# Kernel tuning notes

Measured on AMD Instinct MI355X. Metric: run time of the kernel, lower is better.

Reference implementation:

```python
import jax, jax.numpy as jnp
import numpy as np

NUM_NODES = 100000
NODE_FEAT_DIM = 512
EDGE_FEAT_DIM = 512
MEM_DIM = NODE_FEAT_DIM + EDGE_FEAT_DIM  # 1024
BATCH = 65536


def setup_inputs() -> dict:
    key = jax.random.key(0)
    k_ids, k_mem, k_emb, kq, ks, kk = jax.random.split(key, 6)
    scale = 1.0 / np.sqrt(MEM_DIM)
    inp = {
        "node_ids": jax.random.randint(k_ids, (BATCH,), 0, NUM_NODES, dtype=jnp.int64)
        if jax.config.jax_enable_x64 else
        jax.random.randint(k_ids, (BATCH,), 0, NUM_NODES, dtype=jnp.int32),
        # memory bank: (N, 1, D); randomized (instead of the zero init) so math is non-trivial
        "node_memories": jax.random.normal(k_mem, (NUM_NODES, 1, MEM_DIM), dtype=jnp.float32) * 0.02,
        "node_embedding": jax.random.normal(k_emb, (NUM_NODES, MEM_DIM), dtype=jnp.float32) * 0.02,
        "Wq": jax.random.normal(jax.random.fold_in(kq, 0), (MEM_DIM, NODE_FEAT_DIM), dtype=jnp.float32) * scale,
        "bq": jnp.zeros((NODE_FEAT_DIM,), dtype=jnp.float32),
        "Ws": jax.random.normal(jax.random.fold_in(ks, 0), (MEM_DIM, NODE_FEAT_DIM), dtype=jnp.float32) * scale,
        "bs": jnp.zeros((NODE_FEAT_DIM,), dtype=jnp.float32),
        "Wk": jax.random.normal(jax.random.fold_in(kk, 0), (MEM_DIM, NODE_FEAT_DIM), dtype=jnp.float32) * scale,
        "bk": jnp.zeros((NODE_FEAT_DIM,), dtype=jnp.float32),
    }
    return inp


def reference(node_ids, node_memories, node_embedding, Wq, bq, Ws, bs, Wk, bk):
    ids = node_ids.astype(jnp.int32)
    # torch.sum(node_memories[ids], dim=2): reduces feature dim -> (B, 1)
    mem_sum = jnp.sum(node_memories[ids], axis=2)          # (B, 1)
    x = mem_sum + node_embedding[ids]                      # broadcast -> (B, D)
    q = jax.nn.sigmoid(x @ Wq + bq)                        # (B, node_feat_dim)
    s = jax.nn.sigmoid(x @ Ws + bs)
    k = jax.nn.sigmoid(x @ Wk + bk)
    return (q, s, k)
```

## Files before the change

kernel.cpp:

```cpp
#include <hip/hip_runtime.h>
#include <hip/hip_bf16.h>
#include <stdint.h>

#define BATCH_N 65536
#define KDIM 1024
#define NTOT 1536

typedef __bf16 bf16x8 __attribute__((ext_vector_type(8)));
typedef float f32x4 __attribute__((ext_vector_type(4)));

__device__ __forceinline__ unsigned short f2bf(float f) {
    unsigned u = __builtin_bit_cast(unsigned, f);
    u += 0x7FFFu + ((u >> 16) & 1u);
    return (unsigned short)(u >> 16);
}

__global__ __launch_bounds__(256) void prep_kernel(
    const int* __restrict__ ids,
    const float* __restrict__ mem,
    const float* __restrict__ emb,
    unsigned short* __restrict__ x)
{
    const int b    = blockIdx.x * 4 + (threadIdx.x >> 6);
    const int lane = threadIdx.x & 63;
    const int id   = ids[b];
    const float4* m4 = (const float4*)(mem + (size_t)id * KDIM) + lane;
    const float4* e4 = (const float4*)(emb + (size_t)id * KDIM) + lane;
    float4 v0 = m4[0];
    float4 v1 = m4[64];
    float4 v2 = m4[128];
    float4 v3 = m4[192];
    float s = (v0.x + v0.y + v0.z + v0.w) + (v1.x + v1.y + v1.z + v1.w)
            + (v2.x + v2.y + v2.z + v2.w) + (v3.x + v3.y + v3.z + v3.w);
    #pragma unroll
    for (int off = 1; off < 64; off <<= 1) s += __shfl_xor(s, off, 64);
    unsigned short* xb = x + (size_t)b * KDIM;
    #pragma unroll
    for (int q = 0; q < 4; ++q) {
        float4 e = e4[q * 64];
        ushort4 o;
        o.x = f2bf(s + e.x);
        o.y = f2bf(s + e.y);
        o.z = f2bf(s + e.z);
        o.w = f2bf(s + e.w);
        const int k   = q * 256 + lane * 4;
        const int ksw = k ^ ((b & 7) << 3);
        *(ushort4*)(xb + ksw) = o;
    }
}

__global__ __launch_bounds__(256) void wconv_kernel(
    const float* __restrict__ Wq, const float* __restrict__ Ws,
    const float* __restrict__ Wk, unsigned short* __restrict__ wt)
{
    const int gt = blockIdx.x * 256 + threadIdx.x;
    const int n  = gt % NTOT;
    const int kb = (gt / NTOT) * 4;
    const float* W = (n < 512) ? Wq : ((n < 1024) ? Ws : Wk);
    const int nn = n & 511;
    ushort4 o;
    o.x = f2bf(W[(size_t)(kb + 0) * 512 + nn]);
    o.y = f2bf(W[(size_t)(kb + 1) * 512 + nn]);
    o.z = f2bf(W[(size_t)(kb + 2) * 512 + nn]);
    o.w = f2bf(W[(size_t)(kb + 3) * 512 + nn]);
    const int ksw = kb ^ ((n & 7) << 3);
    *(ushort4*)(wt + (size_t)n * KDIM + ksw) = o;
}

#define BM 256
#define BN 256
#define BK 64
#define MT (BATCH_N / BM)
#define NT (NTOT / BN)
#define NWG (MT * NT)

#define BAR() asm volatile("s_barrier" ::: "memory")
#define LGKM0() asm volatile("s_waitcnt lgkmcnt(0)" ::: "memory")
#define VM6() asm volatile("s_waitcnt vmcnt(6)" ::: "memory")
#define VM0() asm volatile("s_waitcnt vmcnt(0)" ::: "memory")
#define AS1 __attribute__((address_space(1)))
#define AS3 __attribute__((address_space(3)))

__global__ __launch_bounds__(512, 2) void gemm_kernel(
    const unsigned short* __restrict__ X,
    const unsigned short* __restrict__ Wt,
    const float* __restrict__ bq, const float* __restrict__ bs,
    const float* __restrict__ bk, float* __restrict__ out)
{
    __shared__ __align__(16) unsigned short sA[32768];
    __shared__ __align__(16) unsigned short sB[32768];

    const int tid  = threadIdx.x;
    const int xcd  = blockIdx.x & 7;
    const int idx  = blockIdx.x >> 3;
    const int wgid = xcd * (NWG / 8) + idx;
    const int nt   = wgid % NT;
    const int mt   = wgid / NT;
    const int m0   = mt * BM;
    const int n0   = nt * BN;
    const int wid  = tid >> 6;
    const int lane = tid & 63;
    const int wm   = wid >> 2;
    const int wn   = wid & 3;
    const int r16  = lane & 15;
    const int kb0  = (lane >> 4) << 4;
    const int ksw  = (r16 & 7) << 4;

    f32x4 acc[8][4];
    #pragma unroll
    for (int i = 0; i < 8; i++)
        #pragma unroll
        for (int j = 0; j < 4; j++)
            acc[i][j] = f32x4{0.f, 0.f, 0.f, 0.f};

    bf16x8 af[4][2], bfr0[2][2], bfr1[2][2];

    const unsigned short* gA = X  + (size_t)(m0 + (tid >> 3)) * KDIM + (tid & 7) * 8;
    const unsigned short* gB = Wt + (size_t)(n0 + (tid >> 3)) * KDIM + (tid & 7) * 8;
    const int ldst = (tid & 448) * 8;

#define STG_A(slot, h, kt) do {                                                 \
    _Pragma("unroll")                                                            \
    for (int c = 0; c < 2; ++c)                                                  \
        __builtin_amdgcn_global_load_lds(                                        \
            (const AS1 void*)(gA + (size_t)((h) * 128 + c * 64) * KDIM + (kt) * BK), \
            (AS3 void*)(&sA[((slot) * 2 + (h)) * 8192 + c * 4096 + ldst]),       \
            16, 0, 0);                                                           \
} while (0)
#define STG_B(slot, h, kt) do {                                                 \
    _Pragma("unroll")                                                            \
    for (int c = 0; c < 2; ++c)                                                  \
        __builtin_amdgcn_global_load_lds(                                        \
            (const AS1 void*)(gB + (size_t)((h) * 128 + c * 64) * KDIM + (kt) * BK), \
            (AS3 void*)(&sB[((slot) * 2 + (h)) * 8192 + c * 4096 + ldst]),       \
            16, 0, 0);                                                           \
} while (0)

#define LDA(slot, qa) do {                                                      \
    const char* p = (const char*)&sA[((slot) * 2 + (qa)) * 8192];                \
    _Pragma("unroll")                                                            \
    for (int i = 0; i < 4; ++i)                                                  \
        _Pragma("unroll")                                                        \
        for (int kk = 0; kk < 2; ++kk)                                           \
            af[i][kk] = *(const bf16x8*)(p + (wm * 64 + i * 16 + r16) * 128      \
                                           + ((kk * 64 + kb0) ^ ksw));           \
} while (0)
#define LDB(slot, qb, SET) do {                                                 \
    const char* p = (const char*)&sB[((slot) * 2 + (qb)) * 8192];                \
    _Pragma("unroll")                                                            \
    for (int j = 0; j < 2; ++j)                                                  \
        _Pragma("unroll")                                                        \
        for (int kk = 0; kk < 2; ++kk)                                           \
            SET[j][kk] = *(const bf16x8*)(p + (wn * 32 + j * 16 + r16) * 128     \
                                            + ((kk * 64 + kb0) ^ ksw));          \
} while (0)

#define MM(QA, QB, SET) do {                                                    \
    __builtin_amdgcn_s_setprio(1);                                               \
    _Pragma("unroll")                                                            \
    for (int i = 0; i < 4; ++i)                                                  \
        _Pragma("unroll")                                                        \
        for (int j = 0; j < 2; ++j)                                              \
            _Pragma("unroll")                                                    \
            for (int kk = 0; kk < 2; ++kk)                                       \
                acc[(QA) * 4 + i][(QB) * 2 + j] =                                \
                    __builtin_amdgcn_mfma_f32_16x16x32_bf16(                     \
                        af[i][kk], SET[j][kk], acc[(QA) * 4 + i][(QB) * 2 + j],  \
                        0, 0, 0);                                                \
    __builtin_amdgcn_s_setprio(0);                                               \
} while (0)

    STG_A(0, 0, 0); STG_A(0, 1, 0); STG_B(0, 0, 0); STG_B(0, 1, 0);
    STG_A(1, 0, 1); STG_B(1, 1, 1); STG_A(1, 1, 1);
    VM0();
    BAR();

    #pragma unroll 1
    for (int t = 0; t < 7; ++t) {
        const int ka = 2 * t + 1, kb2 = 2 * t + 2, kc = 2 * t + 3;
        LDA(0, 0); LDB(0, 0, bfr0); STG_B(1, 0, ka);
        BAR(); LGKM0(); MM(0, 0, bfr0); BAR();
        LDB(0, 1, bfr1); STG_A(0, 0, kb2);
        BAR(); LGKM0(); MM(0, 1, bfr1); BAR();
        LDA(0, 1); STG_B(0, 1, kb2);
        BAR(); LGKM0(); MM(1, 1, bfr1); BAR();
        STG_A(0, 1, kb2);
        BAR(); LGKM0(); MM(1, 0, bfr0); VM6(); BAR();
        LDA(1, 0); LDB(1, 0, bfr0); STG_B(0, 0, kb2);
        BAR(); LGKM0(); MM(0, 0, bfr0); BAR();
        LDB(1, 1, bfr1); STG_A(1, 0, kc);
        BAR(); LGKM0(); MM(0, 1, bfr1); BAR();
        LDA(1, 1); STG_B(1, 1, kc);
        BAR(); LGKM0(); MM(1, 1, bfr1); BAR();
        STG_A(1, 1, kc);
        BAR(); LGKM0(); MM(1, 0, bfr0); VM6(); BAR();
    }
    LDA(0, 0); LDB(0, 0, bfr0); STG_B(1, 0, 15);
    BAR(); LGKM0(); MM(0, 0, bfr0); BAR();
    LDB(0, 1, bfr1);
    BAR(); LGKM0(); MM(0, 1, bfr1); BAR();
    LDA(0, 1);
    BAR(); LGKM0(); MM(1, 1, bfr1); BAR();
    BAR(); LGKM0(); MM(1, 0, bfr0); VM0(); BAR();
    LDA(1, 0); LDB(1, 0, bfr0);
    BAR(); LGKM0(); MM(0, 0, bfr0); BAR();
    LDB(1, 1, bfr1);
    BAR(); LGKM0(); MM(0, 1, bfr1); BAR();
    LDA(1, 1);
    BAR(); LGKM0(); MM(1, 1, bfr1); BAR();
    BAR(); LGKM0(); MM(1, 0, bfr0);

    const int grp = nt >> 1;
    const float* bias = (grp == 0) ? bq : ((grp == 1) ? bs : bk);
    float* obase = out + (size_t)grp * ((size_t)BATCH_N * 512);
    const int cb = (nt & 1) * 256;
    #pragma unroll
    for (int qb = 0; qb < 2; ++qb)
        #pragma unroll
        for (int j = 0; j < 2; ++j) {
            const int col = cb + qb * 128 + wn * 32 + j * 16 + r16;
            const float bv = bias[col];
            #pragma unroll
            for (int qa = 0; qa < 2; ++qa)
                #pragma unroll
                for (int i = 0; i < 4; ++i) {
                    const int rbase = m0 + qa * 128 + wm * 64 + i * 16 + ((lane >> 4) << 2);
                    #pragma unroll
                    for (int r = 0; r < 4; ++r) {
                        float v = acc[qa * 4 + i][qb * 2 + j][r] + bv;
                        v = 1.0f / (1.0f + __expf(-v));
                        __builtin_nontemporal_store(v, &obase[(size_t)(rbase + r) * 512 + col]);
                    }
                }
        }
#undef STG_A
#undef STG_B
#undef LDA
#undef LDB
#undef MM
}

extern "C" void kernel_launch(void* const* d_in, const int* in_sizes, int n_in,
                              void* d_out, int out_size, void* d_ws, size_t ws_size,
                              hipStream_t stream) {
    const int*   ids = (const int*)d_in[0];
    const float* mem = (const float*)d_in[1];
    const float* emb = (const float*)d_in[2];
    const float* Wq  = (const float*)d_in[3];
    const float* bq  = (const float*)d_in[4];
    const float* Ws  = (const float*)d_in[5];
    const float* bs  = (const float*)d_in[6];
    const float* Wk  = (const float*)d_in[7];
    const float* bk  = (const float*)d_in[8];
    float* out = (float*)d_out;

    unsigned short* x  = (unsigned short*)d_ws;
    unsigned short* wt = x + (size_t)BATCH_N * KDIM;

    hipLaunchKernelGGL(wconv_kernel, dim3(NTOT), dim3(256), 0, stream, Wq, Ws, Wk, wt);
    hipLaunchKernelGGL(prep_kernel, dim3(BATCH_N / 4), dim3(256), 0, stream, ids, mem, emb, x);
    hipLaunchKernelGGL(gemm_kernel, dim3(NWG), dim3(512), 0, stream,
                       x, wt, bq, bs, bk, out);
}
```

Before: 393.2 us.

## Double-buffer A fragments and drop explicit LDS waits in GEMM main loop

Splits the A register fragments into two sets (af0/af1) so the next A fragment loads from LDS can be issued while MFMAs on the current set run. It removes the manual lgkmcnt(0) waits and about half the barriers, leaving LDS-read dependencies to the compiler's waitcnt insertion. The goal is to overlap LDS reads with MFMA work and cut synchronisation stalls. The cost is higher VGPR pressure, and with fewer barriers there is a risk of races where async global-to-LDS stores overwrite slots other waves are still reading.

```diff
diff --git a/kernel.cpp b/kernel.cpp
--- a/kernel.cpp
+++ b/kernel.cpp
@@ -75,7 +75,6 @@
 #define NWG (MT * NT)
 
 #define BAR() asm volatile("s_barrier" ::: "memory")
-#define LGKM0() asm volatile("s_waitcnt lgkmcnt(0)" ::: "memory")
 #define VM6() asm volatile("s_waitcnt vmcnt(6)" ::: "memory")
 #define VM0() asm volatile("s_waitcnt vmcnt(0)" ::: "memory")
 #define AS1 __attribute__((address_space(1)))
@@ -113,7 +112,7 @@
         for (int j = 0; j < 4; j++)
             acc[i][j] = f32x4{0.f, 0.f, 0.f, 0.f};
 
-    bf16x8 af[4][2], bfr0[2][2], bfr1[2][2];
+    bf16x8 af0[4][2], af1[4][2], bfr0[2][2], bfr1[2][2];
 
     const unsigned short* gA = X  + (size_t)(m0 + (tid >> 3)) * KDIM + (tid & 7) * 8;
     const unsigned short* gB = Wt + (size_t)(n0 + (tid >> 3)) * KDIM + (tid & 7) * 8;
@@ -136,16 +135,16 @@
             16, 0, 0);                                                           \
 } while (0)
 
-#define LDA(slot, qa) do {                                                      \
+#define LDA(SET, slot, qa) do {                                                 \
     const char* p = (const char*)&sA[((slot) * 2 + (qa)) * 8192];                \
     _Pragma("unroll")                                                            \
     for (int i = 0; i < 4; ++i)                                                  \
         _Pragma("unroll")                                                        \
         for (int kk = 0; kk < 2; ++kk)                                           \
-            af[i][kk] = *(const bf16x8*)(p + (wm * 64 + i * 16 + r16) * 128      \
-                                           + ((kk * 64 + kb0) ^ ksw));           \
-} while (0)
-#define LDB(slot, qb, SET) do {                                                 \
+            SET[i][kk] = *(const bf16x8*)(p + (wm * 64 + i * 16 + r16) * 128     \
+                                            + ((kk * 64 + kb0) ^ ksw));          \
+} while (0)
+#define LDB(SET, slot, qb) do {                                                 \
     const char* p = (const char*)&sB[((slot) * 2 + (qb)) * 8192];                \
     _Pragma("unroll")                                                            \
     for (int j = 0; j < 2; ++j)                                                  \
@@ -155,7 +154,7 @@
                                             + ((kk * 64 + kb0) ^ ksw));          \
 } while (0)
 
-#define MM(QA, QB, SET) do {                                                    \
+#define MM(QA, QB, ASET, BSET) do {                                             \
     __builtin_amdgcn_s_setprio(1);                                               \
     _Pragma("unroll")                                                            \
     for (int i = 0; i < 4; ++i)                                                  \
@@ -165,8 +164,8 @@
             for (int kk = 0; kk < 2; ++kk)                                       \
                 acc[(QA) * 4 + i][(QB) * 2 + j] =                                \
                     __builtin_amdgcn_mfma_f32_16x16x32_bf16(                     \
-                        af[i][kk], SET[j][kk], acc[(QA) * 4 + i][(QB) * 2 + j],  \
-                        0, 0, 0);                                                \
+                        ASET[i][kk], BSET[j][kk],                                \
+                        acc[(QA) * 4 + i][(QB) * 2 + j], 0, 0, 0);               \
     __builtin_amdgcn_s_setprio(0);                                               \
 } while (0)
 
@@ -178,37 +177,33 @@
     #pragma unroll 1
     for (int t = 0; t < 7; ++t) {
         const int ka = 2 * t + 1, kb2 = 2 * t + 2, kc = 2 * t + 3;
-        LDA(0, 0); LDB(0, 0, bfr0); STG_B(1, 0, ka);
-        BAR(); LGKM0(); MM(0, 0, bfr0); BAR();
-        LDB(0, 1, bfr1); STG_A(0, 0, kb2);
-        BAR(); LGKM0(); MM(0, 1, bfr1); BAR();
-        LDA(0, 1); STG_B(0, 1, kb2);
-        BAR(); LGKM0(); MM(1, 1, bfr1); BAR();
-        STG_A(0, 1, kb2);
-        BAR(); LGKM0(); MM(1, 0, bfr0); VM6(); BAR();
-        LDA(1, 0); LDB(1, 0, bfr0); STG_B(0, 0, kb2);
-        BAR(); LGKM0(); MM(0, 0, bfr0); BAR();
-        LDB(1, 1, bfr1); STG_A(1, 0, kc);
-        BAR(); LGKM0(); MM(0, 1, bfr1); BAR();
-        LDA(1, 1); STG_B(1, 1, kc);
-        BAR(); LGKM0(); MM(1, 1, bfr1); BAR();
-        STG_A(1, 1, kc);
-        BAR(); LGKM0(); MM(1, 0, bfr0); VM6(); BAR();
+        LDA(af0, 0, 0); LDB(bfr0, 0, 0);
+        MM(0, 0, af0, bfr0);
+        LDB(bfr1, 0, 1); STG_B(1, 0, ka);                        BAR();
+        MM(0, 1, af0, bfr1);
+        LDA(af1, 0, 1); STG_A(0, 0, kb2);                        BAR();
+        MM(1, 1, af1, bfr1); STG_B(0, 1, kb2);                   BAR();
+        MM(1, 0, af1, bfr0); STG_A(0, 1, kb2); VM6();            BAR();
+        LDA(af0, 1, 0); LDB(bfr0, 1, 0);
+        MM(0, 0, af0, bfr0);
+        LDB(bfr1, 1, 1); STG_B(0, 0, kb2);                       BAR();
+        MM(0, 1, af0, bfr1);
+        LDA(af1, 1, 1); STG_A(1, 0, kc);                         BAR();
+        MM(1, 1, af1, bfr1); STG_B(1, 1, kc);                    BAR();
+        MM(1, 0, af1, bfr0); STG_A(1, 1, kc); VM6();             BAR();
     }
-    LDA(0, 0); LDB(0, 0, bfr0); STG_B(1, 0, 15);
-    BAR(); LGKM0(); MM(0, 0, bfr0); BAR();
-    LDB(0, 1, bfr1);
-    BAR(); LGKM0(); MM(0, 1, bfr1); BAR();
-    LDA(0, 1);
-    BAR(); LGKM0(); MM(1, 1, bfr1); BAR();
-    BAR(); LGKM0(); MM(1, 0, bfr0); VM0(); BAR();
-    LDA(1, 0); LDB(1, 0, bfr0);
-    BAR(); LGKM0(); MM(0, 0, bfr0); BAR();
-    LDB(1, 1, bfr1);
-    BAR(); LGKM0(); MM(0, 1, bfr1); BAR();
-    LDA(1, 1);
-    BAR(); LGKM0(); MM(1, 1, bfr1); BAR();
-    BAR(); LGKM0(); MM(1, 0, bfr0);
+    LDA(af0, 0, 0); LDB(bfr0, 0, 0);
+    MM(0, 0, af0, bfr0);
+    LDB(bfr1, 0, 1); STG_B(1, 0, 15);                            BAR();
+    MM(0, 1, af0, bfr1); LDA(af1, 0, 1);                         BAR();
+    MM(1, 1, af1, bfr1);                                         BAR();
+    MM(1, 0, af1, bfr0); VM0();                                  BAR();
+    LDA(af0, 1, 0); LDB(bfr0, 1, 0);
+    MM(0, 0, af0, bfr0);
+    LDB(bfr1, 1, 1);                                             BAR();
+    MM(0, 1, af0, bfr1); LDA(af1, 1, 1);                         BAR();
+    MM(1, 1, af1, bfr1);                                         BAR();
+    MM(1, 0, af1, bfr0);
 
     const int grp = nt >> 1;
     const float* bias = (grp == 0) ? bq : ((grp == 1) ? bs : bk);
```

After: 391.3 us. Within noise of the previous version (-0.5%).
